# Kernel optimization log

Measured on AMD Instinct MI355X. Metric: run time of the kernel, lower is better.

The kernel has to match this reference:

```python
import jax, jax.numpy as jnp
import numpy as np

N_NODES = 50000
N_EDGES = 800000
F_DIM = 35   # num_features = in_channels = out_channels
K_HOPS = 3   # num_filters (diffusion order)


def _dconv(xcat, src, dst, w_fwd, w_bwd, theta, bias, n):
    """Dual-direction diffusion convolution: sum_k T_fwd^k X theta[0,k] + T_bwd^k X theta[1,k] + b.
    xcat: [n, Cin]; theta: [2, K, Cin, Cout]; w_fwd/w_bwd: [E] normalized edge weights."""
    out = xcat @ (theta[0, 0] + theta[1, 0]) + bias  # k=0 term (identity hop)
    xf = xcat
    xb = xcat
    for k in range(1, theta.shape[1]):
        # forward diffusion: aggregate src -> dst with out-degree normalization
        xf = jax.ops.segment_sum(w_fwd[:, None] * xf[src], dst, num_segments=n)
        # backward diffusion: aggregate dst -> src with in-degree normalization
        xb = jax.ops.segment_sum(w_bwd[:, None] * xb[dst], src, num_segments=n)
        out = out + xf @ theta[0, k] + xb @ theta[1, k]
    return out


def _cell(x, h, src, dst, wf, wb, tz, bz, tr, br, tc, bc, n):
    """DCRNN GRU cell with diffusion convolutions as the gate transforms."""
    xh = jnp.concatenate([x, h], axis=-1)  # [n, 2F]
    z = jax.nn.sigmoid(_dconv(xh, src, dst, wf, wb, tz, bz, n))
    r = jax.nn.sigmoid(_dconv(xh, src, dst, wf, wb, tr, br, n))
    c = jnp.tanh(_dconv(jnp.concatenate([x, r * h], axis=-1), src, dst, wf, wb, tc, bc, n))
    return z * h + (1.0 - z) * c


def setup_inputs() -> dict:
    key = jax.random.key(0)
    ks = jax.random.split(key, 12)
    x = jax.random.normal(ks[0], (N_NODES, F_DIM), dtype=jnp.float32)
    edge_index = jax.random.randint(ks[1], (2, N_EDGES), 0, N_NODES)
    edge_weight = jax.random.uniform(ks[2], (N_EDGES,), dtype=jnp.float32)
    cin = 2 * F_DIM
    s = 1.0 / np.sqrt(cin)
    u = lambda k, sh: jax.random.uniform(k, sh, jnp.float32, -s, s)
    theta_z = u(ks[3], (2, K_HOPS, cin, F_DIM)); b_z = u(ks[4], (F_DIM,))
    theta_r = u(ks[5], (2, K_HOPS, cin, F_DIM)); b_r = u(ks[6], (F_DIM,))
    theta_c = u(ks[7], (2, K_HOPS, cin, F_DIM)); b_c = u(ks[8], (F_DIM,))
    sl = 1.0 / np.sqrt(F_DIM)
    W_lin = jax.random.uniform(ks[9], (F_DIM, 1), jnp.float32, -sl, sl)
    b_lin = jax.random.uniform(ks[10], (1,), jnp.float32, -sl, sl)
    return dict(x=x, edge_index=edge_index, edge_weight=edge_weight,
                theta_z=theta_z, b_z=b_z, theta_r=theta_r, b_r=b_r,
                theta_c=theta_c, b_c=b_c, W_lin=W_lin, b_lin=b_lin)


def reference(x, edge_index, edge_weight, theta_z, b_z, theta_r, b_r, theta_c, b_c, W_lin, b_lin):
    n = x.shape[0]
    src, dst = edge_index[0], edge_index[1]
    # learned/normalized adjacency A (forward + backward transition weights)
    deg_out = jax.ops.segment_sum(edge_weight, src, num_segments=n)
    deg_in = jax.ops.segment_sum(edge_weight, dst, num_segments=n)
    wf = edge_weight / jnp.where(deg_out[src] > 0, deg_out[src], 1.0)
    wb = edge_weight / jnp.where(deg_in[dst] > 0, deg_in[dst], 1.0)
    A = jnp.stack([wf, wb])  # [2, E]
    h = jnp.zeros_like(x)
    # recurrent cell called twice (second call reuses hidden state and A)
    h = _cell(x, h, src, dst, wf, wb, theta_z, b_z, theta_r, b_r, theta_c, b_c, n)
    h = _cell(x, h, src, dst, wf, wb, theta_z, b_z, theta_r, b_r, theta_c, b_c, n)
    out = jax.nn.relu(h @ W_lin + b_lin)  # [n, 1]
    return out, A
```

## Files before the change

kernel.cpp:

```cpp
#include <hip/hip_runtime.h>
#include <hip/hip_fp16.h>

#define NF 35
#define HS 36
#define TMAT 2450
#define ZCOLS 384
#define ZUSED 360
#define CCOLS 192
#define CUSED 180


__global__ void degree2_k(const int* __restrict__ src, const int* __restrict__ dst,
                          unsigned int* __restrict__ cntF2, unsigned int* __restrict__ cntB2,
                          int* __restrict__ rankF, int* __restrict__ rankB, int E) {
    int e = blockIdx.x * blockDim.x + threadIdx.x;
    if (e < E) {
        int d = dst[e], s = src[e];
        int shd = (d & 1) * 16, shs = (s & 1) * 16;
        unsigned int o1 = atomicAdd(&cntF2[d >> 1], 1u << shd);
        rankF[e] = (int)((o1 >> shd) & 0xFFFFu);
        unsigned int o2 = atomicAdd(&cntB2[s >> 1], 1u << shs);
        rankB[e] = (int)((o2 >> shs) & 0xFFFFu);
    }
}

__global__ __launch_bounds__(1024) void scan2_k(const unsigned int* __restrict__ cntF2,
                                                const unsigned int* __restrict__ cntB2,
                                                int* __restrict__ rowF,
                                                int* __restrict__ rowB, int n) {
    const unsigned int* cnt = blockIdx.x ? cntB2 : cntF2;
    int* row = blockIdx.x ? rowB : rowF;
    __shared__ int wsum[16];
    __shared__ int carry_s;
    int lane = threadIdx.x & 63, wid = threadIdx.x >> 6;
    if (threadIdx.x == 0) carry_s = 0;
    __syncthreads();
    for (int base = 0; base < n; base += 1024) {
        int i = base + threadIdx.x;
        int v = 0;
        if (i < n) v = (int)((cnt[i >> 1] >> ((i & 1) * 16)) & 0xFFFFu);
        int s = v;
        for (int off = 1; off < 64; off <<= 1) {
            int t = __shfl_up(s, off, 64);
            if (lane >= off) s += t;
        }
        if (lane == 63) wsum[wid] = s;
        __syncthreads();
        if (wid == 0) {
            int t = (lane < 16) ? wsum[lane] : 0;
            int ss = t;
            for (int off = 1; off < 16; off <<= 1) {
                int u = __shfl_up(ss, off, 64);
                if (lane >= off) ss += u;
            }
            if (lane < 16) wsum[lane] = ss - t;
        }
        __syncthreads();
        if (i < n) row[i] = carry_s + wsum[wid] + s - v;
        __syncthreads();
        if (threadIdx.x == 1023) carry_s += wsum[15] + s;
        __syncthreads();
    }
    if (threadIdx.x == 0) row[n] = carry_s;
}

__global__ void scatter2_k(const int* __restrict__ src, const int* __restrict__ dst,
                           const float* __restrict__ w,
                           const int* __restrict__ rankF, const int* __restrict__ rankB,
                           const int* __restrict__ rowF, const int* __restrict__ rowB,
                           int2* __restrict__ pairF, int2* __restrict__ pairB, int E) {
    int e = blockIdx.x * blockDim.x + threadIdx.x;
    if (e < E) {
        int s = src[e], d = dst[e];
        int wb = __float_as_int(w[e]);
        pairF[rowF[d] + rankF[e]] = make_int2(s, wb);
        pairB[rowB[s] + rankB[e]] = make_int2(d, wb);
    }
}

__global__ void segdeg_k(const int* __restrict__ rowF, const int* __restrict__ rowB,
                         const int2* __restrict__ pairF, const int2* __restrict__ pairB,
                         float* __restrict__ deg_in, float* __restrict__ deg_out, int n) {
    int i = blockIdx.x * blockDim.x + threadIdx.x;
    if (i >= n) return;
    float a = 0.f;
    for (int p = rowF[i]; p < rowF[i + 1]; ++p) a += __int_as_float(pairF[p].y);
    deg_in[i] = a;
    float b = 0.f;
    for (int p = rowB[i]; p < rowB[i + 1]; ++p) b += __int_as_float(pairB[p].y);
    deg_out[i] = b;
}

__global__ void norm_k(const int* __restrict__ src, const int* __restrict__ dst,
                       const float* __restrict__ w, const float* __restrict__ deg_out,
                       const float* __restrict__ deg_in,
                       const int2* __restrict__ pairF, const int2* __restrict__ pairB,
                       unsigned int* __restrict__ pFp, unsigned int* __restrict__ pBp,
                       float* __restrict__ wf, float* __restrict__ wb, int E) {
    int e = blockIdx.x * blockDim.x + threadIdx.x;
    if (e >= E) return;
    float ww = w[e];
    float a = deg_out[src[e]];
    float b = deg_in[dst[e]];
    wf[e] = ww / (a > 0.f ? a : 1.f);
    wb[e] = ww / (b > 0.f ? b : 1.f);
    int2 pa = pairF[e];
    float da = deg_out[pa.x];
    float wa = __int_as_float(pa.y) / (da > 0.f ? da : 1.f);
    pFp[e] = (unsigned int)pa.x |
             ((unsigned int)__half_as_ushort(__float2half_rn(wa)) << 16);
    int2 pb = pairB[e];
    float db = deg_in[pb.x];
    float wbv = __int_as_float(pb.y) / (db > 0.f ? db : 1.f);
    pBp[e] = (unsigned int)pb.x |
             ((unsigned int)__half_as_ushort(__float2half_rn(wbv)) << 16);
}


__global__ void pack_k(const float* __restrict__ tz, const float* __restrict__ tr_,
                       const float* __restrict__ tc, const float* __restrict__ bz,
                       const float* __restrict__ br, const float* __restrict__ bc,
                       float* __restrict__ PZ, float* __restrict__ PC) {
    int i = blockIdx.x * 256 + threadIdx.x;
    const int tot1 = 71 * ZCOLS;
    if (i < tot1) {
        int r = i / ZCOLS, j = i - r * ZCOLS;
        int s = j / 36, jl = j - s * 36;
        float v = 0.f;
        if (s < 10 && jl < 35) {
            int zr = s & 1;
            const float* th = zr ? tr_ : tz;
            int grp = s >> 1;
            if (r < 70) {
                if (grp == 0) v = th[r * 35 + jl] + th[3 * TMAT + r * 35 + jl];
                else {
                    int off = (grp == 1) ? 1 : (grp == 2) ? 2 : (grp == 3) ? 4 : 5;
                    v = th[off * TMAT + r * 35 + jl];
                }
            } else if (grp == 0) {
                v = zr ? br[jl] : bz[jl];
            }
        }
        PZ[i] = v;
    } else {
        int i2 = i - tot1;
        if (i2 < 71 * CCOLS) {
            int r = i2 / CCOLS, j = i2 - r * CCOLS;
            int s = j / 36, jl = j - s * 36;
            float v = 0.f;
            if (s < 5 && jl < 35) {
                if (r < 70) {
                    if (s == 0) v = tc[r * 35 + jl] + tc[3 * TMAT + r * 35 + jl];
                    else {
                        int off = (s == 1) ? 1 : (s == 2) ? 2 : (s == 3) ? 4 : 5;
                        v = tc[off * TMAT + r * 35 + jl];
                    }
                } else if (s == 0) v = bc[jl];
            }
            PC[i2] = v;
        }
    }
}


__device__ __forceinline__ uint2 pack4h(float4 a) {
    __half2 lo = __floats2half2_rn(a.x, a.y);
    __half2 hi = __floats2half2_rn(a.z, a.w);
    uint2 r;
    r.x = *(unsigned int*)&lo;
    r.y = *(unsigned int*)&hi;
    return r;
}

__device__ __forceinline__ void fma2h(float* a, unsigned int v, float w) {
    float2 f = __half22float2(*(__half2*)&v);
    a[0] += w * f.x;
    a[1] += w * f.y;
}

__device__ __forceinline__ void fma4u2(float* a, uint2 v, float w) {
    fma2h(a, v.x, w);
    fma2h(a + 2, v.y, w);
}

__device__ __forceinline__ void ld4h(float* a, const char* p) {
    uint2 v = *(const uint2*)p;
    a[0] = 0.f; a[1] = 0.f; a[2] = 0.f; a[3] = 0.f;
    fma4u2(a, v, 1.f);
}

__device__ __forceinline__ void st4h(const float* a, char* p) {
    *(uint2*)p = pack4h(make_float4(a[0], a[1], a[2], a[3]));
}

__device__ __forceinline__ float hw(unsigned int e) {
    return __half2float(__ushort_as_half((unsigned short)(e >> 16)));
}

__device__ __forceinline__ void gath8(float* acc, const char* slab, int off,
                                      const int* __restrict__ rp,
                                      const unsigned int* __restrict__ pp, int row) {
    int p = rp[row], p1 = rp[row + 1];
    for (; p + 3 < p1; p += 4) {
        unsigned int e0 = pp[p], e1 = pp[p + 1], e2 = pp[p + 2], e3 = pp[p + 3];
        uint2 v0 = *(const uint2*)(slab + (size_t)(e0 & 0xFFFFu) * 72 + off);
        uint2 v1 = *(const uint2*)(slab + (size_t)(e1 & 0xFFFFu) * 72 + off);
        uint2 v2 = *(const uint2*)(slab + (size_t)(e2 & 0xFFFFu) * 72 + off);
        uint2 v3 = *(const uint2*)(slab + (size_t)(e3 & 0xFFFFu) * 72 + off);
        fma4u2(acc, v0, hw(e0));
        fma4u2(acc, v1, hw(e1));
        fma4u2(acc, v2, hw(e2));
        fma4u2(acc, v3, hw(e3));
    }
    for (; p < p1; ++p) {
        unsigned int e0 = pp[p];
        uint2 v0 = *(const uint2*)(slab + (size_t)(e0 & 0xFFFFu) * 72 + off);
        fma4u2(acc, v0, hw(e0));
    }
}


template <int WCOLS, int USED>
__device__ __forceinline__ void gemm_store8(const float* sxr, const float* __restrict__ W,
                                            char* OUT, size_t slb, int grow, bool valid,
                                            int wid, int kdim) {
#pragma unroll
    for (int jt = 0; jt < (WCOLS + 127) / 128; ++jt) {
        int j0 = __builtin_amdgcn_readfirstlane(jt * 128 + wid * 16);
        if (j0 >= USED) continue;
        const float4* bw = (const float4*)(W + (size_t)70 * WCOLS + j0);
        float4 a0 = bw[0], a1 = bw[1], a2 = bw[2], a3 = bw[3];
        for (int c = 0; c < kdim; ++c) {
            float v = sxr[c];
            const float4* wr = (const float4*)(W + (size_t)c * WCOLS + j0);
            float4 w0 = wr[0], w1 = wr[1], w2 = wr[2], w3 = wr[3];
            a0.x += v * w0.x; a0.y += v * w0.y; a0.z += v * w0.z; a0.w += v * w0.w;
            a1.x += v * w1.x; a1.y += v * w1.y; a1.z += v * w1.z; a1.w += v * w1.w;
            a2.x += v * w2.x; a2.y += v * w2.y; a2.z += v * w2.z; a2.w += v * w2.w;
            a3.x += v * w3.x; a3.y += v * w3.y; a3.z += v * w3.z; a3.w += v * w3.w;
        }
        if (valid) {
            float4 as[4] = {a0, a1, a2, a3};
#pragma unroll
            for (int g = 0; g < 4; ++g) {
                int jc = j0 + 4 * g;
                if (jc >= USED) break;
                int s = jc / 36, off = jc - s * 36;
                *(uint2*)(OUT + (size_t)s * slb + (size_t)grow * 72 + off * 2) =
                    pack4h(as[g]);
            }
        }
    }
}


template <int H0>
__global__ __launch_bounds__(512) void mm_z_k(const float* __restrict__ x,
                                              const float* __restrict__ h,
                                              const float* __restrict__ W,
                                              char* __restrict__ zS, int n) {
    __shared__ float sx[64 * 73];
    int row0 = blockIdx.x * 64;
    for (int t = threadIdx.x; t < 64 * 35; t += 512) {
        int rl = t / 35, c = t - rl * 35;
        int grow = row0 + rl;
        sx[rl * 73 + c] = (grow < n) ? x[(size_t)grow * 35 + c] : 0.f;
    }
    if (!H0) {
        for (int t = threadIdx.x; t < 64 * 35; t += 512) {
            int rl = t / 35, c = t - rl * 35;
            int grow = row0 + rl;
            sx[rl * 73 + 35 + c] = (grow < n) ? h[(size_t)grow * HS + c] : 0.f;
        }
    }
    __syncthreads();
    int lane = threadIdx.x & 63;
    int wid = threadIdx.x >> 6;
    int grow = row0 + lane;
    gemm_store8<ZCOLS, ZUSED>(&sx[lane * 73], W, zS, (size_t)n * 72, grow, grow < n,
                              wid, H0 ? 35 : 70);
}


__global__ __launch_bounds__(512) void mmc_k(const float* __restrict__ x,
                                             const float* __restrict__ h,
                                             const char* __restrict__ zS,
                                             const float* __restrict__ W,
                                             char* __restrict__ cS, int n) {
    __shared__ float sx[64 * 73];
    size_t slb = (size_t)n * 72;
    int row0 = blockIdx.x * 64;
    for (int t = threadIdx.x; t < 64 * 35; t += 512) {
        int rl = t / 35, c = t - rl * 35;
        int grow = row0 + rl;
        sx[rl * 73 + c] = (grow < n) ? x[(size_t)grow * 35 + c] : 0.f;
    }
    for (int t = threadIdx.x; t < 64 * 35; t += 512) {
        int rl = t / 35, c = t - rl * 35;
        int grow = row0 + rl;
        float v = 0.f;
        if (grow < n) {
            float r = __half2float(*(const __half*)(zS + slb + (size_t)grow * 72 + 2 * c));
            v = r * h[(size_t)grow * HS + c];
        }
        sx[rl * 73 + 35 + c] = v;
    }
    __syncthreads();
    int lane = threadIdx.x & 63;
    int wid = threadIdx.x >> 6;
    int grow = row0 + lane;
    gemm_store8<CCOLS, CUSED>(&sx[lane * 73], W, cS, slb, grow, grow < n, wid, 70);
}


__global__ __launch_bounds__(256) void hopAz_k(char* __restrict__ zS,
                                               const int* __restrict__ rowF,
                                               const int* __restrict__ rowB,
                                               const unsigned int* __restrict__ pF,
                                               const unsigned int* __restrict__ pB,
                                               int n) {
    int i = blockIdx.x * 256 + threadIdx.x;
    if (i >= n * 9) return;
    size_t slb = (size_t)n * 72;
    int pass = blockIdx.y;
    const int* rp = (pass < 2) ? rowF : rowB;
    const unsigned int* pp = (pass < 2) ? pF : pB;
    int dstS = (pass == 0) ? 2 : (pass == 1) ? 3 : (pass == 2) ? 6 : 7;
    int srcS = dstS + 2;
    int row = i / 9, t = i - row * 9;
    int off = 8 * t;
    char* wp = zS + (size_t)dstS * slb + (size_t)row * 72 + off;
    float acc[4];
    ld4h(acc, wp);
    gath8(acc, zS + (size_t)srcS * slb, off, rp, pp, row);
    st4h(acc, wp);
}

__global__ __launch_bounds__(256) void hopBz_k(char* __restrict__ zS,
                                               const int* __restrict__ rowF,
                                               const int* __restrict__ rowB,
                                               const unsigned int* __restrict__ pF,
                                               const unsigned int* __restrict__ pB,
                                               int n) {
    int i = blockIdx.x * 256 + threadIdx.x;
    if (i >= n * 9) return;
    size_t slb = (size_t)n * 72;
    int g = blockIdx.y;
    int row = i / 9, t = i - row * 9;
    int off = 8 * t;
    char* wp = zS + (size_t)g * slb + (size_t)row * 72 + off;
    float acc[4];
    ld4h(acc, wp);
    gath8(acc, zS + (size_t)(2 + g) * slb, off, rowF, pF, row);
    gath8(acc, zS + (size_t)(6 + g) * slb, off, rowB, pB, row);
#pragma unroll
    for (int k = 0; k < 4; ++k) acc[k] = 1.f / (1.f + expf(-acc[k]));
    st4h(acc, wp);
}

__global__ __launch_bounds__(256) void hopAc_k(char* __restrict__ cS,
                                               const int* __restrict__ rowF,
                                               const int* __restrict__ rowB,
                                               const unsigned int* __restrict__ pF,
                                               const unsigned int* __restrict__ pB,
                                               int n) {
    int i = blockIdx.x * 256 + threadIdx.x;
    if (i >= n * 9) return;
    size_t slb = (size_t)n * 72;
    int pass = blockIdx.y;
    const int* rp = pass ? rowB : rowF;
    const unsigned int* pp = pass ? pB : pF;
    int dstS = pass ? 3 : 1;
    int srcS = pass ? 4 : 2;
    int row = i / 9, t = i - row * 9;
    int off = 8 * t;
    char* wp = cS + (size_t)dstS * slb + (size_t)row * 72 + off;
    float acc[4];
    ld4h(acc, wp);
    gath8(acc, cS + (size_t)srcS * slb, off, rp, pp, row);
    st4h(acc, wp);
}

__global__ __launch_bounds__(256) void hopBcg_k(const char* __restrict__ cS,
                                                const char* __restrict__ zS,
                                                const int* __restrict__ rowF,
                                                const int* __restrict__ rowB,
                                                const unsigned int* __restrict__ pF,
                                                const unsigned int* __restrict__ pB,
                                                float* __restrict__ h, int n) {
    int i = blockIdx.x * 256 + threadIdx.x;
    if (i >= n * 9) return;
    size_t slb = (size_t)n * 72;
    int row = i / 9, t = i - row * 9;
    int off = 8 * t;
    float acc[4];
    ld4h(acc, cS + (size_t)row * 72 + off);
    gath8(acc, cS + slb, off, rowF, pF, row);
    gath8(acc, cS + 3 * slb, off, rowB, pB, row);
    float zv[4];
    ld4h(zv, zS + (size_t)row * 72 + off);
    float* hp = h + (size_t)row * HS + 4 * t;
    float4 h4 = *(float4*)hp;
    float hv[4] = {h4.x, h4.y, h4.z, h4.w};
#pragma unroll
    for (int k = 0; k < 4; ++k) {
        float c = tanhf(acc[k]);
        hv[k] = zv[k] * hv[k] + (1.f - zv[k]) * c;
    }
    *(float4*)hp = make_float4(hv[0], hv[1], hv[2], hv[3]);
}


__global__ void final_k(const float* __restrict__ h, const float* __restrict__ Wl,
                        const float* __restrict__ bl, float* __restrict__ out, int n) {
    int i = blockIdx.x * blockDim.x + threadIdx.x;
    if (i < n) {
        float s = bl[0];
        const float* hr = h + (size_t)i * HS;
#pragma unroll
        for (int j = 0; j < NF; j++) s += hr[j] * Wl[j];
        out[i] = fmaxf(s, 0.f);
    }
}


extern "C" void kernel_launch(void* const* d_in, const int* in_sizes, int n_in,
                              void* d_out, int out_size, void* d_ws, size_t ws_size,
                              hipStream_t stream) {
    const float* x   = (const float*)d_in[0];
    const int*   ei  = (const int*)d_in[1];
    const float* w   = (const float*)d_in[2];
    const float* tz  = (const float*)d_in[3];
    const float* bz  = (const float*)d_in[4];
    const float* tr_ = (const float*)d_in[5];
    const float* br  = (const float*)d_in[6];
    const float* tc  = (const float*)d_in[7];
    const float* bc  = (const float*)d_in[8];
    const float* Wl  = (const float*)d_in[9];
    const float* bl  = (const float*)d_in[10];

    const int n = in_sizes[0] / NF;
    const int E = in_sizes[2];
    const int* src = ei;
    const int* dst = ei + E;

    float* out = (float*)d_out;
    float* wf = out + n;
    float* wb = wf + E;

    char* p = (char*)d_ws;
    auto alloc = [&](size_t bytes) {
        char* r = p;
        p += (bytes + 15) & ~(size_t)15;
        return r;
    };
    int2* pairF = (int2*)alloc((size_t)E * 8);
    int2* pairB = (int2*)alloc((size_t)E * 8);
    unsigned int* pFp = (unsigned int*)alloc((size_t)E * 4);
    unsigned int* pBp = (unsigned int*)alloc((size_t)E * 4);
    int* rowF = (int*)alloc((size_t)(n + 1) * 4);
    int* rowB = (int*)alloc((size_t)(n + 1) * 4);
    unsigned int* cntF2 = (unsigned int*)alloc((size_t)((n + 1) / 2 + 4) * 4);
    unsigned int* cntB2 = (unsigned int*)alloc((size_t)((n + 1) / 2 + 4) * 4);
    float* deg_in  = (float*)alloc((size_t)n * 4);
    float* deg_out = (float*)alloc((size_t)n * 4);
    float* h  = (float*)alloc((size_t)n * HS * 4);
    char* zS  = alloc((size_t)n * 72 * 10);
    char* cS  = alloc((size_t)n * 72 * 5);
    float* PZ = (float*)alloc((size_t)71 * ZCOLS * 4);
    float* PC = (float*)alloc((size_t)71 * CCOLS * 4);
    int* rankF = (int*)zS;
    int* rankB = rankF + E;

    const int gridE = (E + 255) / 256;
    const int gridN = (n + 255) / 256;
    const int g64 = (n + 63) / 64;
    const int g9 = (n * 9 + 255) / 256;
    const size_t cntBytes = ((size_t)((n + 1) / 2 + 4) * 4 + 15) & ~(size_t)15;

    hipMemsetAsync(cntF2, 0, 2 * cntBytes, stream);
    hipMemsetAsync(h, 0, (size_t)n * HS * sizeof(float), stream);
    degree2_k<<<gridE, 256, 0, stream>>>(src, dst, cntF2, cntB2, rankF, rankB, E);
    scan2_k<<<2, 1024, 0, stream>>>(cntF2, cntB2, rowF, rowB, n);
    scatter2_k<<<gridE, 256, 0, stream>>>(src, dst, w, rankF, rankB, rowF, rowB,
                                          pairF, pairB, E);
    segdeg_k<<<gridN, 256, 0, stream>>>(rowF, rowB, pairF, pairB, deg_in, deg_out, n);
    norm_k<<<gridE, 256, 0, stream>>>(src, dst, w, deg_out, deg_in, pairF, pairB,
                                      pFp, pBp, wf, wb, E);
    pack_k<<<(71 * (ZCOLS + CCOLS) + 255) / 256, 256, 0, stream>>>(tz, tr_, tc,
                                                                   bz, br, bc, PZ, PC);

    mm_z_k<1><<<g64, 512, 0, stream>>>(x, h, PZ, zS, n);
    hopAz_k<<<dim3(g9, 4), 256, 0, stream>>>(zS, rowF, rowB, pFp, pBp, n);
    hopBz_k<<<dim3(g9, 2), 256, 0, stream>>>(zS, rowF, rowB, pFp, pBp, n);
    mmc_k<<<g64, 512, 0, stream>>>(x, h, zS, PC, cS, n);
    hopAc_k<<<dim3(g9, 2), 256, 0, stream>>>(cS, rowF, rowB, pFp, pBp, n);
    hopBcg_k<<<g9, 256, 0, stream>>>(cS, zS, rowF, rowB, pFp, pBp, h, n);
    mm_z_k<0><<<g64, 512, 0, stream>>>(x, h, PZ, zS, n);
    hopAz_k<<<dim3(g9, 4), 256, 0, stream>>>(zS, rowF, rowB, pFp, pBp, n);
    hopBz_k<<<dim3(g9, 2), 256, 0, stream>>>(zS, rowF, rowB, pFp, pBp, n);
    mmc_k<<<g64, 512, 0, stream>>>(x, h, zS, PC, cS, n);
    hopAc_k<<<dim3(g9, 2), 256, 0, stream>>>(cS, rowF, rowB, pFp, pBp, n);
    hopBcg_k<<<g9, 256, 0, stream>>>(cS, zS, rowF, rowB, pFp, pBp, h, n);

    final_k<<<gridN, 256, 0, stream>>>(h, Wl, bl, out, n);
}
```

Baseline: 619.7 us.

## Split final hop gathers per direction and add separate combine kernels

The final-hop kernels that gathered both forward and backward neighbours in one thread are split into separate per-direction passes launched over a 2D grid. Their partial results go to scratch slabs, and new lightweight kernels sum them and apply the sigmoid or the GRU tanh update. The gather loop also gets an 8-way unrolled path so more loads are in flight per thread. The aim is more parallelism and memory-level concurrency in the gathers, at the cost of extra launches and extra slab reads and writes.

```diff
diff --git a/kernel.cpp b/kernel.cpp
--- a/kernel.cpp
+++ b/kernel.cpp
@@ -201,6 +201,22 @@
                                       const int* __restrict__ rp,
                                       const unsigned int* __restrict__ pp, int row) {
     int p = rp[row], p1 = rp[row + 1];
+    for (; p + 7 < p1; p += 8) {
+        unsigned int e0 = pp[p], e1 = pp[p + 1], e2 = pp[p + 2], e3 = pp[p + 3];
+        unsigned int e4 = pp[p + 4], e5 = pp[p + 5], e6 = pp[p + 6], e7 = pp[p + 7];
+        uint2 v0 = *(const uint2*)(slab + (size_t)(e0 & 0xFFFFu) * 72 + off);
+        uint2 v1 = *(const uint2*)(slab + (size_t)(e1 & 0xFFFFu) * 72 + off);
+        uint2 v2 = *(const uint2*)(slab + (size_t)(e2 & 0xFFFFu) * 72 + off);
+        uint2 v3 = *(const uint2*)(slab + (size_t)(e3 & 0xFFFFu) * 72 + off);
+        uint2 v4 = *(const uint2*)(slab + (size_t)(e4 & 0xFFFFu) * 72 + off);
+        uint2 v5 = *(const uint2*)(slab + (size_t)(e5 & 0xFFFFu) * 72 + off);
+        uint2 v6 = *(const uint2*)(slab + (size_t)(e6 & 0xFFFFu) * 72 + off);
+        uint2 v7 = *(const uint2*)(slab + (size_t)(e7 & 0xFFFFu) * 72 + off);
+        fma4u2(acc, v0, hw(e0)); fma4u2(acc, v1, hw(e1));
+        fma4u2(acc, v2, hw(e2)); fma4u2(acc, v3, hw(e3));
+        fma4u2(acc, v4, hw(e4)); fma4u2(acc, v5, hw(e5));
+        fma4u2(acc, v6, hw(e6)); fma4u2(acc, v7, hw(e7));
+    }
     for (; p + 3 < p1; p += 4) {
         unsigned int e0 = pp[p], e1 = pp[p + 1], e2 = pp[p + 2], e3 = pp[p + 3];
         uint2 v0 = *(const uint2*)(slab + (size_t)(e0 & 0xFFFFu) * 72 + off);
@@ -336,26 +352,51 @@
     st4h(acc, wp);
 }
 
-__global__ __launch_bounds__(256) void hopBz_k(char* __restrict__ zS,
-                                               const int* __restrict__ rowF,
-                                               const int* __restrict__ rowB,
-                                               const unsigned int* __restrict__ pF,
-                                               const unsigned int* __restrict__ pB,
-                                               int n) {
+__global__ __launch_bounds__(256) void hopBzp_k(char* __restrict__ zS,
+                                                const int* __restrict__ rowF,
+                                                const int* __restrict__ rowB,
+                                                const unsigned int* __restrict__ pF,
+                                                const unsigned int* __restrict__ pB,
+                                                int n) {
     int i = blockIdx.x * 256 + threadIdx.x;
     if (i >= n * 9) return;
     size_t slb = (size_t)n * 72;
-    int g = blockIdx.y;
+    int pass = blockIdx.y;
+    int gate = pass & 1;
+    int dir = pass >> 1;
+    const int* rp = dir ? rowB : rowF;
+    const unsigned int* pp = dir ? pB : pF;
+    int srcS = (dir ? 6 : 2) + gate;
+    int dstS = srcS + 2;
     int row = i / 9, t = i - row * 9;
     int off = 8 * t;
-    char* wp = zS + (size_t)g * slb + (size_t)row * 72 + off;
     float acc[4];
-    ld4h(acc, wp);
-    gath8(acc, zS + (size_t)(2 + g) * slb, off, rowF, pF, row);
-    gath8(acc, zS + (size_t)(6 + g) * slb, off, rowB, pB, row);
+    if (dir == 0) {
+        ld4h(acc, zS + (size_t)gate * slb + (size_t)row * 72 + off);
+    } else {
+        acc[0] = 0.f; acc[1] = 0.f; acc[2] = 0.f; acc[3] = 0.f;
+    }
+    gath8(acc, zS + (size_t)srcS * slb, off, rp, pp, row);
+    st4h(acc, zS + (size_t)dstS * slb + (size_t)row * 72 + off);
+}
+
+__global__ __launch_bounds__(256) void sigcomb_k(char* __restrict__ zS, int n) {
+    int i = blockIdx.x * 256 + threadIdx.x;
+    if (i >= n * 9) return;
+    size_t slb = (size_t)n * 72;
+    int row = i / 9, t = i - row * 9;
+    size_t base = (size_t)row * 72 + 8 * t;
+    float a[4], b[4];
+    ld4h(a, zS + 4 * slb + base);
+    ld4h(b, zS + 8 * slb + base);
 #pragma unroll
-    for (int k = 0; k < 4; ++k) acc[k] = 1.f / (1.f + expf(-acc[k]));
-    st4h(acc, wp);
+    for (int k = 0; k < 4; ++k) a[k] = 1.f / (1.f + expf(-(a[k] + b[k])));
+    st4h(a, zS + base);
+    ld4h(a, zS + 5 * slb + base);
+    ld4h(b, zS + 9 * slb + base);
+#pragma unroll
+    for (int k = 0; k < 4; ++k) a[k] = 1.f / (1.f + expf(-(a[k] + b[k])));
+    st4h(a, zS + slb + base);
 }
 
 __global__ __launch_bounds__(256) void hopAc_k(char* __restrict__ cS,
@@ -381,30 +422,50 @@
     st4h(acc, wp);
 }
 
-__global__ __launch_bounds__(256) void hopBcg_k(const char* __restrict__ cS,
-                                                const char* __restrict__ zS,
+__global__ __launch_bounds__(256) void hopBcp_k(char* __restrict__ cS,
                                                 const int* __restrict__ rowF,
                                                 const int* __restrict__ rowB,
                                                 const unsigned int* __restrict__ pF,
                                                 const unsigned int* __restrict__ pB,
-                                                float* __restrict__ h, int n) {
+                                                int n) {
     int i = blockIdx.x * 256 + threadIdx.x;
     if (i >= n * 9) return;
     size_t slb = (size_t)n * 72;
+    int pass = blockIdx.y;
+    const int* rp = pass ? rowB : rowF;
+    const unsigned int* pp = pass ? pB : pF;
+    int srcS = pass ? 3 : 1;
+    int dstS = pass ? 4 : 2;
     int row = i / 9, t = i - row * 9;
     int off = 8 * t;
     float acc[4];
-    ld4h(acc, cS + (size_t)row * 72 + off);
-    gath8(acc, cS + slb, off, rowF, pF, row);
-    gath8(acc, cS + 3 * slb, off, rowB, pB, row);
-    float zv[4];
-    ld4h(zv, zS + (size_t)row * 72 + off);
+    if (pass == 0) {
+        ld4h(acc, cS + (size_t)row * 72 + off);
+    } else {
+        acc[0] = 0.f; acc[1] = 0.f; acc[2] = 0.f; acc[3] = 0.f;
+    }
+    gath8(acc, cS + (size_t)srcS * slb, off, rp, pp, row);
+    st4h(acc, cS + (size_t)dstS * slb + (size_t)row * 72 + off);
+}
+
+__global__ __launch_bounds__(256) void grucomb_k(const char* __restrict__ cS,
+                                                 const char* __restrict__ zS,
+                                                 float* __restrict__ h, int n) {
+    int i = blockIdx.x * 256 + threadIdx.x;
+    if (i >= n * 9) return;
+    size_t slb = (size_t)n * 72;
+    int row = i / 9, t = i - row * 9;
+    size_t base = (size_t)row * 72 + 8 * t;
+    float a[4], b[4], zv[4];
+    ld4h(a, cS + 2 * slb + base);
+    ld4h(b, cS + 4 * slb + base);
+    ld4h(zv, zS + base);
     float* hp = h + (size_t)row * HS + 4 * t;
     float4 h4 = *(float4*)hp;
     float hv[4] = {h4.x, h4.y, h4.z, h4.w};
 #pragma unroll
     for (int k = 0; k < 4; ++k) {
-        float c = tanhf(acc[k]);
+        float c = tanhf(a[k] + b[k]);
         hv[k] = zv[k] * hv[k] + (1.f - zv[k]) * c;
     }
     *(float4*)hp = make_float4(hv[0], hv[1], hv[2], hv[3]);
@@ -490,18 +551,19 @@
     pack_k<<<(71 * (ZCOLS + CCOLS) + 255) / 256, 256, 0, stream>>>(tz, tr_, tc,
                                                                    bz, br, bc, PZ, PC);
 
-    mm_z_k<1><<<g64, 512, 0, stream>>>(x, h, PZ, zS, n);
-    hopAz_k<<<dim3(g9, 4), 256, 0, stream>>>(zS, rowF, rowB, pFp, pBp, n);
-    hopBz_k<<<dim3(g9, 2), 256, 0, stream>>>(zS, rowF, rowB, pFp, pBp, n);
-    mmc_k<<<g64, 512, 0, stream>>>(x, h, zS, PC, cS, n);
-    hopAc_k<<<dim3(g9, 2), 256, 0, stream>>>(cS, rowF, rowB, pFp, pBp, n);
-    hopBcg_k<<<g9, 256, 0, stream>>>(cS, zS, rowF, rowB, pFp, pBp, h, n);
-    mm_z_k<0><<<g64, 512, 0, stream>>>(x, h, PZ, zS, n);
-    hopAz_k<<<dim3(g9, 4), 256, 0, stream>>>(zS, rowF, rowB, pFp, pBp, n);
-    hopBz_k<<<dim3(g9, 2), 256, 0, stream>>>(zS, rowF, rowB, pFp, pBp, n);
-    mmc_k<<<g64, 512, 0, stream>>>(x, h, zS, PC, cS, n);
-    hopAc_k<<<dim3(g9, 2), 256, 0, stream>>>(cS, rowF, rowB, pFp, pBp, n);
-    hopBcg_k<<<g9, 256, 0, stream>>>(cS, zS, rowF, rowB, pFp, pBp, h, n);
+    for (int cellit = 0; cellit < 2; ++cellit) {
+        if (cellit == 0)
+            mm_z_k<1><<<g64, 512, 0, stream>>>(x, h, PZ, zS, n);
+        else
+            mm_z_k<0><<<g64, 512, 0, stream>>>(x, h, PZ, zS, n);
+        hopAz_k<<<dim3(g9, 4), 256, 0, stream>>>(zS, rowF, rowB, pFp, pBp, n);
+        hopBzp_k<<<dim3(g9, 4), 256, 0, stream>>>(zS, rowF, rowB, pFp, pBp, n);
+        sigcomb_k<<<g9, 256, 0, stream>>>(zS, n);
+        mmc_k<<<g64, 512, 0, stream>>>(x, h, zS, PC, cS, n);
+        hopAc_k<<<dim3(g9, 2), 256, 0, stream>>>(cS, rowF, rowB, pFp, pBp, n);
+        hopBcp_k<<<dim3(g9, 2), 256, 0, stream>>>(cS, rowF, rowB, pFp, pBp, n);
+        grucomb_k<<<g9, 256, 0, stream>>>(cS, zS, h, n);
+    }
 
     final_k<<<gridN, 256, 0, stream>>>(h, Wl, bl, out, n);
 }
```

Measured after the change: 627.9 us. About the same (+1.3%).
